# Optimization experiments

Measured on AMD Instinct MI355X. Metric: run time of the kernel, lower is better.

Reference implementation:

```python
import jax, jax.numpy as jnp
import numpy as np

N = 100000   # nodes
E = 1600000  # edges
D = 128      # input_dim
H = 128      # hidden_dim
G = 64       # graphs in batch
L = 3        # num GCN layers
BN_EPS = 1e-5


def setup_inputs() -> dict:
    key = jax.random.key(0)
    ks = jax.random.split(key, 16)
    s = 1.0 / np.sqrt(H)
    inp = {
        "x": jax.random.normal(ks[0], (N, D), jnp.float32),
        "edge_index": jax.random.randint(ks[1], (2, E), 0, N, dtype=jnp.int64),
        "batch": jnp.sort(jax.random.randint(ks[2], (N,), 0, G, dtype=jnp.int64)),
        # stacked GCNConv params (input_dim == hidden_dim so layer 0 stacks too)
        "conv_w": jax.random.normal(ks[3], (L, H, H), jnp.float32) * s,
        "conv_b": jax.random.normal(ks[4], (L, H), jnp.float32) * 0.01,
        # BatchNorm1d running stats + affine (eval mode)
        "bn_gamma": jnp.ones((L, H), jnp.float32),
        "bn_beta": jnp.zeros((L, H), jnp.float32),
        "bn_mean": jax.random.normal(ks[5], (L, H), jnp.float32) * 0.1,
        "bn_var": jax.random.uniform(ks[6], (L, H), jnp.float32, 0.5, 1.5),
        # node head MLP
        "node_w1": jax.random.normal(ks[7], (H // 2, H), jnp.float32) * s,
        "node_b1": jnp.zeros((H // 2,), jnp.float32),
        "node_w2": jax.random.normal(ks[8], (2, H // 2), jnp.float32) * (1.0 / np.sqrt(H // 2)),
        "node_b2": jnp.zeros((2,), jnp.float32),
        # graph head MLP
        "graph_w1": jax.random.normal(ks[9], (H // 2, H), jnp.float32) * s,
        "graph_b1": jnp.zeros((H // 2,), jnp.float32),
        "graph_w2": jax.random.normal(ks[10], (2, H // 2), jnp.float32) * (1.0 / np.sqrt(H // 2)),
        "graph_b2": jnp.zeros((2,), jnp.float32),
    }
    return inp


def _gcn_layer(h, src, dst, deg_inv_sqrt, w, b):
    # PyG GCNConv: h' = W h, then symmetric-normalized scatter-add over
    # edges (self-loops already appended to src/dst).
    h = h @ w.T                                   # [N, H]
    norm = deg_inv_sqrt[src] * deg_inv_sqrt[dst]  # [E+N]
    msg = h[src] * norm[:, None]                  # [E+N, H] gather
    out = jax.ops.segment_sum(msg, dst, num_segments=N)  # scatter-add
    return out + b


def _forward(x, edge_index, batch, conv_w, conv_b, bn_gamma, bn_beta,
             bn_mean, bn_var, node_w1, node_b1, node_w2, node_b2,
             graph_w1, graph_b1, graph_w2, graph_b2):
    loops = jnp.arange(N, dtype=edge_index.dtype)
    src = jnp.concatenate([edge_index[0], loops])
    dst = jnp.concatenate([edge_index[1], loops])
    deg = jax.ops.segment_sum(jnp.ones_like(src, dtype=x.dtype), dst,
                              num_segments=N)
    deg_inv_sqrt = jnp.where(deg > 0, jax.lax.rsqrt(deg), 0.0)

    h = x
    for i in range(L):  # conv -> BN(eval) -> ReLU (dropout inactive in eval)
        h = _gcn_layer(h, src, dst, deg_inv_sqrt, conv_w[i], conv_b[i])
        h = (h - bn_mean[i]) * jax.lax.rsqrt(bn_var[i] + BN_EPS) * bn_gamma[i] + bn_beta[i]
        h = jax.nn.relu(h)

    node_pred = jax.nn.relu(h @ node_w1.T + node_b1) @ node_w2.T + node_b2

    counts = jax.ops.segment_sum(jnp.ones((N,), h.dtype), batch,
                                 num_segments=G)
    graph_emb = jax.ops.segment_sum(h, batch, num_segments=G) / \
        jnp.maximum(counts, 1.0)[:, None]
    graph_pred = jax.nn.relu(graph_emb @ graph_w1.T + graph_b1) @ graph_w2.T + graph_b2
    return node_pred, graph_pred


def reference(x, edge_index, batch, conv_w, conv_b, bn_gamma, bn_beta,
              bn_mean, bn_var, node_w1, node_b1, node_w2, node_b2,
              graph_w1, graph_b1, graph_w2, graph_b2):
    return _forward(x, edge_index, batch, conv_w, conv_b, bn_gamma, bn_beta,
                    bn_mean, bn_var, node_w1, node_b1, node_w2, node_b2,
                    graph_w1, graph_b1, graph_w2, graph_b2)
```

## Files before the change

### kernel.cpp

```cpp
#include <hip/hip_runtime.h>
#include <hip/hip_bf16.h>

#define NN 100000
#define EE 1600000
#define HH 128
#define GG 64
#define LL 3
#define BN_EPS 1e-5f
#define NT 391
#define CHW 392
#define CAP 6144

typedef __hip_bfloat16 bf16;
typedef __attribute__((ext_vector_type(8))) short short8;
typedef __attribute__((ext_vector_type(4))) float floatx4;

__device__ __forceinline__ float lo16(unsigned v) { return __uint_as_float(v << 16); }
__device__ __forceinline__ float hi16(unsigned v) { return __uint_as_float(v & 0xffff0000u); }
__device__ __forceinline__ unsigned short f2b(float v) {
    bf16 h = __float2bfloat16(v);
    return *(unsigned short*)&h;
}
__device__ __forceinline__ unsigned pack2(float a, float b) {
    return (unsigned)f2b(a) | ((unsigned)f2b(b) << 16);
}
__device__ __forceinline__ int geti(const int* __restrict__ p, int i, int f) {
    return f ? p[2 * i] : p[i];
}

__global__ __launch_bounds__(1024) void k_part(const int* __restrict__ ei,
        unsigned* __restrict__ chunk, unsigned short* __restrict__ lbu,
        int* __restrict__ flag,
        const float* __restrict__ conv_w, const float* __restrict__ nw1,
        unsigned short* __restrict__ cwB, unsigned short* __restrict__ n1B,
        float* __restrict__ bnA, float* __restrict__ bnB,
        const float* __restrict__ conv_b, const float* __restrict__ g,
        const float* __restrict__ be, const float* __restrict__ mn,
        const float* __restrict__ vr, float* __restrict__ gsum,
        float* __restrict__ gcnt, unsigned* __restrict__ tbz) {
    __shared__ int lcnt[NT];
    __shared__ int wsum[8];
    __shared__ unsigned short lbs[CHW];
    __shared__ unsigned sorted[4096];
    int t = threadIdx.x;
    int e0 = blockIdx.x * 4096;
    int probe = ei[2 * (e0 + (t & 63)) + 1];
    int f = __any(probe != 0) ? 0 : 1;
    if (blockIdx.x == 0 && t == 0) *flag = f;
    int gi = blockIdx.x * 1024 + t;
    if (gi < LL * HH * HH) cwB[gi] = f2b(conv_w[gi]);
    if (gi < 64 * HH) n1B[gi] = f2b(nw1[gi]);
    if (gi < LL * HH) {
        float A = g[gi] * rsqrtf(vr[gi] + BN_EPS);
        bnA[gi] = A;
        bnB[gi] = (conv_b[gi] - mn[gi]) * A + be[gi];
    }
    if (gi < GG * HH) gsum[gi] = 0.f;
    if (gi < GG) gcnt[gi] = 0.f;
    if (gi < 64) tbz[(size_t)NN * 64 + gi] = 0u;
    int nume = EE - e0 < 4096 ? EE - e0 : 4096;
    for (int i = t; i < NT; i += 1024) lcnt[i] = 0;
    __syncthreads();
    unsigned pk[4]; int ml[4], mt[4];
#pragma unroll
    for (int i = 0; i < 4; i++) {
        int li = i * 1024 + t;
        if (li < nume) {
            int e = e0 + li;
            int src = geti(ei, e, f), dst = geti(ei, EE + e, f);
            mt[i] = dst >> 8;
            pk[i] = ((unsigned)src << 8) | (unsigned)(dst & 255);
            ml[i] = atomicAdd(&lcnt[mt[i]], 1);
        }
    }
    __syncthreads();
    int own = 0, x = 0;
    if (t < 512) { own = t < NT ? lcnt[t] : 0; x = own; }
#pragma unroll
    for (int off = 1; off < 64; off <<= 1) {
        int y = __shfl_up(x, off);
        if ((t & 63) >= off) x += y;
    }
    if (t < 512 && (t & 63) == 63) wsum[t >> 6] = x;
    __syncthreads();
    if (t < NT) {
        int pre = 0, w = t >> 6;
#pragma unroll
        for (int i = 0; i < 7; i++) if (i < w) pre += wsum[i];
        lbs[t] = (unsigned short)(pre + x - own);
    }
    if (t == 0) lbs[NT] = (unsigned short)nume;
    __syncthreads();
#pragma unroll
    for (int i = 0; i < 4; i++) {
        int li = i * 1024 + t;
        if (li < nume) sorted[(int)lbs[mt[i]] + ml[i]] = pk[i];
    }
    if (t < CHW) lbu[blockIdx.x * CHW + t] = lbs[t];
    __syncthreads();
    for (int idx = t; idx < nume; idx += 1024)
        chunk[e0 + idx] = sorted[idx];
}

__global__ __launch_bounds__(1024) void k_csr(const unsigned* __restrict__ chunk,
        const unsigned short* __restrict__ lbu, unsigned* __restrict__ csr,
        int* __restrict__ offs, int* __restrict__ cnt, float* __restrict__ dinv) {
    __shared__ unsigned stage[CAP];
    __shared__ unsigned outb[CAP];
    __shared__ int wsum[8];
    __shared__ int w2[4];
    __shared__ int segso[512];
    __shared__ int segst[512];
    __shared__ int hist[256], cur[256];
    __shared__ int s_nep;
    int T = blockIdx.x, t = threadIdx.x;
    int st = 0, rl = 0;
    if (t < NT) {
        int s0 = lbu[t * CHW + T];
        int s1 = lbu[t * CHW + T + 1];
        st = t * 4096 + s0;
        rl = s1 - s0;
    }
    int x = (t < 512) ? rl : 0;
#pragma unroll
    for (int off = 1; off < 64; off <<= 1) {
        int y = __shfl_up(x, off);
        if ((t & 63) >= off) x += y;
    }
    if (t < 512 && (t & 63) == 63) wsum[t >> 6] = x;
    if (t < 256) hist[t] = 0;
    __syncthreads();
    int tot = 0;
#pragma unroll
    for (int i = 0; i < 8; i++) tot += wsum[i];
    int ne = tot > CAP ? CAP : tot;
    if (t < 512) {
        int pre = 0, w = t >> 6;
#pragma unroll
        for (int i = 0; i < 7; i++) if (i < w) pre += wsum[i];
        segso[t] = pre + x - rl;
        segst[t] = st;
    }
    __syncthreads();
    for (int i = t; i < ne; i += 1024) {
        int lo = 0;
#pragma unroll
        for (int b = 256; b; b >>= 1) {
            int nlo = lo + b;
            if (nlo < 512 && segso[nlo] <= i) lo = nlo;
        }
        stage[i] = chunk[segst[lo] + (i - segso[lo])];
    }
    __syncthreads();
    for (int i = t; i < ne; i += 1024)
        atomicAdd(&hist[stage[i] & 255u], 1);
    __syncthreads();
    int c = 0, pc = 0, x2 = 0;
    if (t < 256) {
        c = hist[t];
        pc = (c + 7) & ~7;
        x2 = pc;
    }
#pragma unroll
    for (int off = 1; off < 64; off <<= 1) {
        int y = __shfl_up(x2, off);
        if ((t & 63) >= off) x2 += y;
    }
    if (t < 256 && (t & 63) == 63) w2[t >> 6] = x2;
    __syncthreads();
    if (t < 256) {
        int pre = 0, w = t >> 6;
#pragma unroll
        for (int i = 0; i < 3; i++) if (i < w) pre += w2[i];
        int stn = pre + x2 - pc;
        cur[t] = stn;
        int node = T * 256 + t;
        if (node < NN) {
            offs[node] = T * CAP + stn;
            cnt[node] = c;
            dinv[node] = rsqrtf(1.0f + (float)c);
        }
        for (int i = stn + c; i < stn + pc && i < CAP; i++)
            outb[i] = NN;
    }
    if (t == 0) {
        int tt = w2[0] + w2[1] + w2[2] + w2[3];
        s_nep = tt < CAP ? tt : CAP;
    }
    __syncthreads();
    for (int i = t; i < ne; i += 1024) {
        unsigned p = stage[i];
        int q = atomicAdd(&cur[p & 255u], 1);
        if (q < CAP) outb[q] = p >> 8;
    }
    __syncthreads();
    int nep = s_nep;
    for (int i = t; i < nep; i += 1024)
        csr[(size_t)T * CAP + i] = outb[i];
}

template<typename AT, int NC, bool FUSE>
__global__ __launch_bounds__(256) void k_gemm(const AT* __restrict__ in,
        const unsigned short* __restrict__ Wb, const float* __restrict__ bias,
        unsigned short* __restrict__ outh, int do_relu,
        const float* __restrict__ scale,
        const float* __restrict__ w2, const float* __restrict__ b2v,
        float* __restrict__ out2f) {
    __shared__ char sB[NC * 272];
    int wave = threadIdx.x >> 6, lane = threadIdx.x & 63;
    int ln = lane & 15, q = lane >> 4;
    {
        const short8* wsrc = (const short8*)Wb;
        for (int i = threadIdx.x; i < NC * 16; i += 256) {
            short8 v = wsrc[i];
            *(short8*)(sB + (i >> 4) * 272 + (i & 15) * 16) = v;
        }
    }
    int r0 = blockIdx.x * 64 + wave * 16;
    int row = r0 + ln;
    int rr = row < NN ? row : NN - 1;
    short8 a[4];
    if constexpr (sizeof(AT) == 2) {
        const short8* ap = (const short8*)(in + (size_t)rr * HH);
#pragma unroll
        for (int kt = 0; kt < 4; kt++) a[kt] = ap[kt * 4 + q];
    } else {
        const float4* ap = (const float4*)(in + (size_t)rr * HH);
#pragma unroll
        for (int kt = 0; kt < 4; kt++) {
            float4 f0 = ap[(kt * 4 + q) * 2];
            float4 f1 = ap[(kt * 4 + q) * 2 + 1];
            a[kt][0] = (short)f2b(f0.x); a[kt][1] = (short)f2b(f0.y);
            a[kt][2] = (short)f2b(f0.z); a[kt][3] = (short)f2b(f0.w);
            a[kt][4] = (short)f2b(f1.x); a[kt][5] = (short)f2b(f1.y);
            a[kt][6] = (short)f2b(f1.z); a[kt][7] = (short)f2b(f1.w);
        }
    }
    float scl[4];
    if constexpr (!FUSE) {
#pragma unroll
        for (int reg = 0; reg < 4; reg++) {
            int orow = r0 + q * 4 + reg;
            scl[reg] = scale ? scale[orow < NN ? orow : NN - 1] : 1.f;
        }
    }
    __syncthreads();
    float p0[4], p1[4];
    if constexpr (FUSE) {
#pragma unroll
        for (int r = 0; r < 4; r++) { p0[r] = 0.f; p1[r] = 0.f; }
    }
#pragma unroll
    for (int ct = 0; ct < NC / 16; ct++) {
        int c = ct * 16 + ln;
        floatx4 acc = {0.f, 0.f, 0.f, 0.f};
#pragma unroll
        for (int kt = 0; kt < 4; kt++) {
            short8 b = *(const short8*)(sB + (size_t)c * 272 + kt * 64 + q * 16);
            acc = __builtin_amdgcn_mfma_f32_16x16x32_bf16(a[kt], b, acc, 0, 0, 0);
        }
        float bv = bias ? bias[c] : 0.f;
        if constexpr (FUSE) {
            float wa = w2[c], wb = w2[64 + c];
#pragma unroll
            for (int reg = 0; reg < 4; reg++) {
                float v = fmaxf(acc[reg] + bv, 0.f);
                p0[reg] = fmaf(v, wa, p0[reg]);
                p1[reg] = fmaf(v, wb, p1[reg]);
            }
        } else {
#pragma unroll
            for (int reg = 0; reg < 4; reg++) {
                int orow = r0 + q * 4 + reg;
                if (orow < NN) {
                    float v = acc[reg] + bv;
                    if (do_relu) v = fmaxf(v, 0.f);
                    outh[(size_t)orow * NC + c] = f2b(v * scl[reg]);
                }
            }
        }
    }
    if constexpr (FUSE) {
#pragma unroll
        for (int off = 1; off < 16; off <<= 1) {
#pragma unroll
            for (int r = 0; r < 4; r++) {
                p0[r] += __shfl_xor(p0[r], off);
                p1[r] += __shfl_xor(p1[r], off);
            }
        }
        if (ln == 0) {
            float ba = b2v[0], bb = b2v[1];
#pragma unroll
            for (int reg = 0; reg < 4; reg++) {
                int orow = r0 + q * 4 + reg;
                if (orow < NN)
                    ((float2*)out2f)[orow] = make_float2(p0[reg] + ba, p1[reg] + bb);
            }
        }
    }
}

__global__ __launch_bounds__(256) void k_aggr(const unsigned* __restrict__ tbs,
        const unsigned* __restrict__ csr, const int* __restrict__ offs,
        const int* __restrict__ cnt, const float* __restrict__ dinv,
        const float* __restrict__ bnA, const float* __restrict__ bnB,
        unsigned* __restrict__ hout) {
    int wave = threadIdx.x >> 6, lane = threadIdx.x & 63;
    int n0 = blockIdx.x * 8 + wave * 2;
    int n1 = n0 + 1;
    int base0 = __builtin_amdgcn_readfirstlane(offs[n0]);
    int base1 = __builtin_amdgcn_readfirstlane(offs[n1]);
    int ne0   = __builtin_amdgcn_readfirstlane(cnt[n0]);
    int ne1   = __builtin_amdgcn_readfirstlane(cnt[n1]);
    float dd0 = __uint_as_float(__builtin_amdgcn_readfirstlane(
                    (int)__float_as_uint(dinv[n0])));
    float dd1 = __uint_as_float(__builtin_amdgcn_readfirstlane(
                    (int)__float_as_uint(dinv[n1])));
    unsigned sv0 = tbs[(size_t)n0 * 64 + lane];
    unsigned sv1 = tbs[(size_t)n1 * 64 + lane];
    float ax0 = lo16(sv0), ay0 = hi16(sv0);
    float ax1 = lo16(sv1), ay1 = hi16(sv1);
    const unsigned* __restrict__ e0 = csr + base0;
    const unsigned* __restrict__ e1 = csr + base1;
    int nr0 = (ne0 + 7) & ~7, nr1 = (ne1 + 7) & ~7;
    int nr = nr0 > nr1 ? nr0 : nr1;
    for (int k0 = 0; k0 < nr; k0 += 8) {
        unsigned vv0[8], vv1[8];
        bool a0 = k0 < nr0, a1 = k0 < nr1;
        if (a0) {
#pragma unroll
            for (int j = 0; j < 8; j++) {
                int s = (int)e0[k0 + j];
                vv0[j] = tbs[(size_t)s * 64 + lane];
            }
        }
        if (a1) {
#pragma unroll
            for (int j = 0; j < 8; j++) {
                int s = (int)e1[k0 + j];
                vv1[j] = tbs[(size_t)s * 64 + lane];
            }
        }
        if (a0) {
#pragma unroll
            for (int j = 0; j < 8; j++) {
                ax0 += lo16(vv0[j]);
                ay0 += hi16(vv0[j]);
            }
        }
        if (a1) {
#pragma unroll
            for (int j = 0; j < 8; j++) {
                ax1 += lo16(vv1[j]);
                ay1 += hi16(vv1[j]);
            }
        }
    }
    float2 A = ((const float2*)bnA)[lane];
    float2 B = ((const float2*)bnB)[lane];
    float r0 = fmaxf(fmaf(ax0 * dd0, A.x, B.x), 0.f);
    float r1 = fmaxf(fmaf(ay0 * dd0, A.y, B.y), 0.f);
    float r2 = fmaxf(fmaf(ax1 * dd1, A.x, B.x), 0.f);
    float r3 = fmaxf(fmaf(ay1 * dd1, A.y, B.y), 0.f);
    hout[(size_t)n0 * 64 + lane] = pack2(r0, r1);
    hout[(size_t)n1 * 64 + lane] = pack2(r2, r3);
}

#define PN 32
__global__ __launch_bounds__(64) void k_pool(const unsigned* __restrict__ hb,
        const int* __restrict__ batch, float* __restrict__ gsum,
        float* __restrict__ gcnt, const int* __restrict__ flag) {
    int lane = threadIdx.x;
    int f = *flag;
    int s0 = blockIdx.x * PN;
    int cur = geti(batch, s0, f);
    float a0 = 0.f, a1 = 0.f, cn = 0.f;
    auto step = [&](int g, unsigned v) {
        if (g != cur) {
            atomicAdd(&gsum[cur * HH + 2 * lane], a0);
            atomicAdd(&gsum[cur * HH + 2 * lane + 1], a1);
            if (lane == 0) atomicAdd(&gcnt[cur], cn);
            a0 = a1 = cn = 0.f; cur = g;
        }
        a0 += lo16(v); a1 += hi16(v); cn += 1.f;
    };
    for (int n = s0; n < s0 + PN; n += 8) {
        int gg[8]; unsigned vv[8];
#pragma unroll
        for (int j = 0; j < 8; j++) {
            gg[j] = geti(batch, n + j, f);
            vv[j] = hb[(size_t)(n + j) * 64 + lane];
        }
#pragma unroll
        for (int j = 0; j < 8; j++) step(gg[j], vv[j]);
    }
    atomicAdd(&gsum[cur * HH + 2 * lane], a0);
    atomicAdd(&gsum[cur * HH + 2 * lane + 1], a1);
    if (lane == 0) atomicAdd(&gcnt[cur], cn);
}

__global__ __launch_bounds__(64) void k_ghead(const float* __restrict__ gsum,
        const float* __restrict__ gcnt, const float* __restrict__ w1,
        const float* __restrict__ b1, const float* __restrict__ w2,
        const float* __restrict__ b2v, float* __restrict__ out) {
    __shared__ float emb[HH];
    __shared__ float w1s[64 * 129];
    int g = blockIdx.x, lane = threadIdx.x;
    for (int gi = lane; gi < 64 * HH; gi += 64)
        w1s[(gi >> 7) * 129 + (gi & 127)] = w1[gi];
    float cn = gcnt[g];
    cn = cn > 1.f ? cn : 1.f;
    float inv = 1.f / cn;
    emb[lane] = gsum[g * HH + lane] * inv;
    emb[lane + 64] = gsum[g * HH + 64 + lane] * inv;
    __syncthreads();
    float acc = b1[lane];
    for (int k = 0; k < HH; k++) acc = fmaf(emb[k], w1s[lane * 129 + k], acc);
    float y = fmaxf(acc, 0.f);
    float v0 = y * w2[lane];
    float v1 = y * w2[64 + lane];
#pragma unroll
    for (int off = 32; off; off >>= 1) {
        v0 += __shfl_xor(v0, off);
        v1 += __shfl_xor(v1, off);
    }
    if (lane == 0) {
        out[(size_t)NN * 2 + g * 2]     = v0 + b2v[0];
        out[(size_t)NN * 2 + g * 2 + 1] = v1 + b2v[1];
    }
}

extern "C" void kernel_launch(void* const* d_in, const int* in_sizes, int n_in,
                              void* d_out, int out_size, void* d_ws, size_t ws_size,
                              hipStream_t stream) {
    const float* x      = (const float*)d_in[0];
    const int*   ei     = (const int*)d_in[1];
    const int*   batch  = (const int*)d_in[2];
    const float* conv_w = (const float*)d_in[3];
    const float* conv_b = (const float*)d_in[4];
    const float* bn_g   = (const float*)d_in[5];
    const float* bn_b   = (const float*)d_in[6];
    const float* bn_m   = (const float*)d_in[7];
    const float* bn_v   = (const float*)d_in[8];
    const float* nw1    = (const float*)d_in[9];
    const float* nb1    = (const float*)d_in[10];
    const float* nw2    = (const float*)d_in[11];
    const float* nb2    = (const float*)d_in[12];
    const float* gw1    = (const float*)d_in[13];
    const float* gb1    = (const float*)d_in[14];
    const float* gw2    = (const float*)d_in[15];
    const float* gb2    = (const float*)d_in[16];
    float* out = (float*)d_out;

    char* ws = (char*)d_ws;
    size_t off = 0;
    auto alloc = [&](size_t bytes) -> void* {
        void* p = ws + off;
        off += (bytes + 255) & ~(size_t)255;
        return p;
    };
    unsigned short* hb   = (unsigned short*)alloc((size_t)NN * HH * 2);
    unsigned short* tb   = (unsigned short*)alloc((size_t)(NN + 1) * HH * 2);
    unsigned* chunk  = (unsigned*)alloc((size_t)EE * 4);
    unsigned* csr    = (unsigned*)alloc((size_t)NT * CAP * 4);
    unsigned short* lbu = (unsigned short*)alloc((size_t)NT * CHW * 2);
    int*      offs   = (int*)     alloc((size_t)NN * 4);
    int*      cnt    = (int*)     alloc((size_t)NN * 4);
    float*    dinv   = (float*)   alloc((size_t)NN * 4);
    float*    bnA    = (float*)   alloc((size_t)LL * HH * 4);
    float*    bnB    = (float*)   alloc((size_t)LL * HH * 4);
    float*    gsum   = (float*)   alloc((size_t)GG * HH * 4);
    float*    gcnt   = (float*)   alloc((size_t)GG * 4);
    unsigned short* cwB = (unsigned short*)alloc((size_t)LL * HH * HH * 2);
    unsigned short* n1B = (unsigned short*)alloc((size_t)64 * HH * 2);
    int*      flag   = (int*)     alloc(256);

    k_part<<<NT, 1024, 0, stream>>>(ei, chunk, lbu, flag, conv_w, nw1, cwB, n1B,
            bnA, bnB, conv_b, bn_g, bn_b, bn_m, bn_v, gsum, gcnt, (unsigned*)tb);
    k_csr<<<NT, 1024, 0, stream>>>(chunk, lbu, csr, offs, cnt, dinv);

    k_gemm<float, HH, false><<<(NN + 63) / 64, 256, 0, stream>>>(
        x, cwB, nullptr, tb, 0, dinv, nullptr, nullptr, nullptr);
    k_aggr<<<NN / 8, 256, 0, stream>>>((const unsigned*)tb, csr, offs, cnt,
                                       dinv, bnA, bnB, (unsigned*)hb);
    for (int l = 1; l < LL; l++) {
        k_gemm<unsigned short, HH, false><<<(NN + 63) / 64, 256, 0, stream>>>(
            hb, cwB + (size_t)l * HH * HH, nullptr, tb, 0, dinv,
            nullptr, nullptr, nullptr);
        k_aggr<<<NN / 8, 256, 0, stream>>>((const unsigned*)tb, csr, offs,
                                           cnt, dinv, bnA + l * HH,
                                           bnB + l * HH, (unsigned*)hb);
    }

    k_gemm<unsigned short, 64, true><<<(NN + 63) / 64, 256, 0, stream>>>(
        hb, n1B, nb1, nullptr, 1, nullptr, nw2, nb2, out);

    k_pool<<<(NN + PN - 1) / PN, 64, 0, stream>>>((const unsigned*)hb, batch,
                                                  gsum, gcnt, flag);
    k_ghead<<<GG, 64, 0, stream>>>(gsum, gcnt, gw1, gb1, gw2, gb2, out);
}
```

Measured before the change: 411.4 us.

## Fuse all pipeline stages into one cooperative persistent kernel with grid syncs

Replaces the sequence of separate launches (partition, CSR build, per-layer GEMM and aggregation, node head, pooling, graph head) with a single cooperative kernel. The phases are separated by grid-wide barriers and each phase grid-strides over its tiles. The aim is to remove per-launch overhead and the gaps between kernels. In exchange it adds grid-sync cost, moves GEMM tiles to 1024-thread blocks, and sets a launch bound of 8 blocks of 1024 threads per CU. That bound can force a very low register budget and cause spills, and the phases lose per-kernel tuning.

```diff
diff --git a/kernel.cpp b/kernel.cpp
--- a/kernel.cpp
+++ b/kernel.cpp
@@ -1,5 +1,8 @@
 #include <hip/hip_runtime.h>
 #include <hip/hip_bf16.h>
+#include <hip/hip_cooperative_groups.h>
+
+namespace cg = cooperative_groups;
 
 #define NN 100000
 #define EE 1600000
@@ -10,6 +13,9 @@
 #define NT 391
 #define CHW 392
 #define CAP 6144
+#define PN 32
+#define NTG 391
+#define SMEM_BYTES 55552
 
 typedef __hip_bfloat16 bf16;
 typedef __attribute__((ext_vector_type(8))) short short8;
@@ -28,430 +34,470 @@
     return f ? p[2 * i] : p[i];
 }
 
-__global__ __launch_bounds__(1024) void k_part(const int* __restrict__ ei,
-        unsigned* __restrict__ chunk, unsigned short* __restrict__ lbu,
-        int* __restrict__ flag,
-        const float* __restrict__ conv_w, const float* __restrict__ nw1,
-        unsigned short* __restrict__ cwB, unsigned short* __restrict__ n1B,
-        float* __restrict__ bnA, float* __restrict__ bnB,
-        const float* __restrict__ conv_b, const float* __restrict__ g,
-        const float* __restrict__ be, const float* __restrict__ mn,
-        const float* __restrict__ vr, float* __restrict__ gsum,
-        float* __restrict__ gcnt, unsigned* __restrict__ tbz) {
-    __shared__ int lcnt[NT];
-    __shared__ int wsum[8];
-    __shared__ unsigned short lbs[CHW];
-    __shared__ unsigned sorted[4096];
+struct MegaArgs {
+    const int* ei; const int* batch; const float* x;
+    const float* conv_w; const float* conv_b;
+    const float* bn_g; const float* bn_b; const float* bn_m; const float* bn_v;
+    const float* nw1; const float* nb1; const float* nw2; const float* nb2;
+    const float* gw1; const float* gb1; const float* gw2; const float* gb2;
+    float* out;
+    unsigned short* hb; unsigned short* tb;
+    unsigned* chunk; unsigned* csr; unsigned short* lbu;
+    int* offs; int* cnt; float* dinv;
+    float* bnA; float* bnB; float* gsum; float* gcnt;
+    unsigned short* cwB; unsigned short* n1B; int* flag;
+};
+
+__device__ void phase_part(char* smem, int NB, int f, const MegaArgs& A) {
+    int* lcnt = (int*)smem;
+    int* wsum = (int*)(smem + 1568);
+    unsigned short* lbs = (unsigned short*)(smem + 1600);
+    unsigned* sorted = (unsigned*)(smem + 2384);
     int t = threadIdx.x;
-    int e0 = blockIdx.x * 4096;
-    int probe = ei[2 * (e0 + (t & 63)) + 1];
-    int f = __any(probe != 0) ? 0 : 1;
-    if (blockIdx.x == 0 && t == 0) *flag = f;
     int gi = blockIdx.x * 1024 + t;
-    if (gi < LL * HH * HH) cwB[gi] = f2b(conv_w[gi]);
-    if (gi < 64 * HH) n1B[gi] = f2b(nw1[gi]);
+    if (gi < LL * HH * HH) A.cwB[gi] = f2b(A.conv_w[gi]);
+    if (gi < 64 * HH) A.n1B[gi] = f2b(A.nw1[gi]);
     if (gi < LL * HH) {
-        float A = g[gi] * rsqrtf(vr[gi] + BN_EPS);
-        bnA[gi] = A;
-        bnB[gi] = (conv_b[gi] - mn[gi]) * A + be[gi];
-    }
-    if (gi < GG * HH) gsum[gi] = 0.f;
-    if (gi < GG) gcnt[gi] = 0.f;
-    if (gi < 64) tbz[(size_t)NN * 64 + gi] = 0u;
-    int nume = EE - e0 < 4096 ? EE - e0 : 4096;
-    for (int i = t; i < NT; i += 1024) lcnt[i] = 0;
-    __syncthreads();
-    unsigned pk[4]; int ml[4], mt[4];
-#pragma unroll
-    for (int i = 0; i < 4; i++) {
-        int li = i * 1024 + t;
-        if (li < nume) {
-            int e = e0 + li;
-            int src = geti(ei, e, f), dst = geti(ei, EE + e, f);
-            mt[i] = dst >> 8;
-            pk[i] = ((unsigned)src << 8) | (unsigned)(dst & 255);
-            ml[i] = atomicAdd(&lcnt[mt[i]], 1);
-        }
-    }
-    __syncthreads();
-    int own = 0, x = 0;
-    if (t < 512) { own = t < NT ? lcnt[t] : 0; x = own; }
-#pragma unroll
-    for (int off = 1; off < 64; off <<= 1) {
-        int y = __shfl_up(x, off);
-        if ((t & 63) >= off) x += y;
-    }
-    if (t < 512 && (t & 63) == 63) wsum[t >> 6] = x;
-    __syncthreads();
-    if (t < NT) {
-        int pre = 0, w = t >> 6;
-#pragma unroll
-        for (int i = 0; i < 7; i++) if (i < w) pre += wsum[i];
-        lbs[t] = (unsigned short)(pre + x - own);
-    }
-    if (t == 0) lbs[NT] = (unsigned short)nume;
-    __syncthreads();
-#pragma unroll
-    for (int i = 0; i < 4; i++) {
-        int li = i * 1024 + t;
-        if (li < nume) sorted[(int)lbs[mt[i]] + ml[i]] = pk[i];
-    }
-    if (t < CHW) lbu[blockIdx.x * CHW + t] = lbs[t];
-    __syncthreads();
-    for (int idx = t; idx < nume; idx += 1024)
-        chunk[e0 + idx] = sorted[idx];
-}
-
-__global__ __launch_bounds__(1024) void k_csr(const unsigned* __restrict__ chunk,
-        const unsigned short* __restrict__ lbu, unsigned* __restrict__ csr,
-        int* __restrict__ offs, int* __restrict__ cnt, float* __restrict__ dinv) {
-    __shared__ unsigned stage[CAP];
-    __shared__ unsigned outb[CAP];
-    __shared__ int wsum[8];
-    __shared__ int w2[4];
-    __shared__ int segso[512];
-    __shared__ int segst[512];
-    __shared__ int hist[256], cur[256];
-    __shared__ int s_nep;
-    int T = blockIdx.x, t = threadIdx.x;
-    int st = 0, rl = 0;
-    if (t < NT) {
-        int s0 = lbu[t * CHW + T];
-        int s1 = lbu[t * CHW + T + 1];
-        st = t * 4096 + s0;
-        rl = s1 - s0;
-    }
-    int x = (t < 512) ? rl : 0;
-#pragma unroll
-    for (int off = 1; off < 64; off <<= 1) {
-        int y = __shfl_up(x, off);
-        if ((t & 63) >= off) x += y;
-    }
-    if (t < 512 && (t & 63) == 63) wsum[t >> 6] = x;
-    if (t < 256) hist[t] = 0;
-    __syncthreads();
-    int tot = 0;
-#pragma unroll
-    for (int i = 0; i < 8; i++) tot += wsum[i];
-    int ne = tot > CAP ? CAP : tot;
-    if (t < 512) {
-        int pre = 0, w = t >> 6;
-#pragma unroll
-        for (int i = 0; i < 7; i++) if (i < w) pre += wsum[i];
-        segso[t] = pre + x - rl;
-        segst[t] = st;
-    }
-    __syncthreads();
-    for (int i = t; i < ne; i += 1024) {
-        int lo = 0;
-#pragma unroll
-        for (int b = 256; b; b >>= 1) {
-            int nlo = lo + b;
-            if (nlo < 512 && segso[nlo] <= i) lo = nlo;
-        }
-        stage[i] = chunk[segst[lo] + (i - segso[lo])];
-    }
-    __syncthreads();
-    for (int i = t; i < ne; i += 1024)
-        atomicAdd(&hist[stage[i] & 255u], 1);
-    __syncthreads();
-    int c = 0, pc = 0, x2 = 0;
-    if (t < 256) {
-        c = hist[t];
-        pc = (c + 7) & ~7;
-        x2 = pc;
-    }
-#pragma unroll
-    for (int off = 1; off < 64; off <<= 1) {
-        int y = __shfl_up(x2, off);
-        if ((t & 63) >= off) x2 += y;
-    }
-    if (t < 256 && (t & 63) == 63) w2[t >> 6] = x2;
-    __syncthreads();
-    if (t < 256) {
-        int pre = 0, w = t >> 6;
-#pragma unroll
-        for (int i = 0; i < 3; i++) if (i < w) pre += w2[i];
-        int stn = pre + x2 - pc;
-        cur[t] = stn;
-        int node = T * 256 + t;
-        if (node < NN) {
-            offs[node] = T * CAP + stn;
-            cnt[node] = c;
-            dinv[node] = rsqrtf(1.0f + (float)c);
-        }
-        for (int i = stn + c; i < stn + pc && i < CAP; i++)
-            outb[i] = NN;
-    }
-    if (t == 0) {
-        int tt = w2[0] + w2[1] + w2[2] + w2[3];
-        s_nep = tt < CAP ? tt : CAP;
-    }
-    __syncthreads();
-    for (int i = t; i < ne; i += 1024) {
-        unsigned p = stage[i];
-        int q = atomicAdd(&cur[p & 255u], 1);
-        if (q < CAP) outb[q] = p >> 8;
-    }
-    __syncthreads();
-    int nep = s_nep;
-    for (int i = t; i < nep; i += 1024)
-        csr[(size_t)T * CAP + i] = outb[i];
+        float Av = A.bn_g[gi] * rsqrtf(A.bn_v[gi] + BN_EPS);
+        A.bnA[gi] = Av;
+        A.bnB[gi] = (A.conv_b[gi] - A.bn_m[gi]) * Av + A.bn_b[gi];
+    }
+    if (gi < GG * HH) A.gsum[gi] = 0.f;
+    if (gi < GG) A.gcnt[gi] = 0.f;
+    if (gi < 64) ((unsigned*)A.tb)[(size_t)NN * 64 + gi] = 0u;
+    if (blockIdx.x == 0 && t == 0) *A.flag = f;
+    for (int T = blockIdx.x; T < NT; T += NB) {
+        int e0 = T * 4096;
+        int nume = EE - e0 < 4096 ? EE - e0 : 4096;
+        for (int i = t; i < NT; i += 1024) lcnt[i] = 0;
+        __syncthreads();
+        unsigned pk[4]; int ml[4], mt[4];
+#pragma unroll
+        for (int i = 0; i < 4; i++) {
+            int li = i * 1024 + t;
+            if (li < nume) {
+                int e = e0 + li;
+                int src = geti(A.ei, e, f), dst = geti(A.ei, EE + e, f);
+                mt[i] = dst >> 8;
+                pk[i] = ((unsigned)src << 8) | (unsigned)(dst & 255);
+                ml[i] = atomicAdd(&lcnt[mt[i]], 1);
+            }
+        }
+        __syncthreads();
+        int own = 0, x = 0;
+        if (t < 512) { own = t < NT ? lcnt[t] : 0; x = own; }
+#pragma unroll
+        for (int off = 1; off < 64; off <<= 1) {
+            int y = __shfl_up(x, off);
+            if ((t & 63) >= off) x += y;
+        }
+        if (t < 512 && (t & 63) == 63) wsum[t >> 6] = x;
+        __syncthreads();
+        if (t < NT) {
+            int pre = 0, w = t >> 6;
+#pragma unroll
+            for (int i = 0; i < 7; i++) if (i < w) pre += wsum[i];
+            lbs[t] = (unsigned short)(pre + x - own);
+        }
+        if (t == 0) lbs[NT] = (unsigned short)nume;
+        __syncthreads();
+#pragma unroll
+        for (int i = 0; i < 4; i++) {
+            int li = i * 1024 + t;
+            if (li < nume) sorted[(int)lbs[mt[i]] + ml[i]] = pk[i];
+        }
+        if (t < CHW) A.lbu[T * CHW + t] = lbs[t];
+        __syncthreads();
+        for (int idx = t; idx < nume; idx += 1024)
+            A.chunk[e0 + idx] = sorted[idx];
+    }
+}
+
+__device__ void phase_csr(char* smem, int NB, const MegaArgs& A) {
+    unsigned* stage = (unsigned*)smem;
+    unsigned* outb  = (unsigned*)(smem + 24576);
+    int* segso = (int*)(smem + 49152);
+    int* segst = (int*)(smem + 51200);
+    int* hist  = (int*)(smem + 53248);
+    int* cur   = (int*)(smem + 54272);
+    int* wsum  = (int*)(smem + 55296);
+    int* w2x   = (int*)(smem + 55328);
+    int* s_nep = (int*)(smem + 55344);
+    int t = threadIdx.x;
+    for (int T = blockIdx.x; T < NT; T += NB) {
+        int st = 0, rl = 0;
+        if (t < NT) {
+            int s0 = A.lbu[t * CHW + T];
+            int s1 = A.lbu[t * CHW + T + 1];
+            st = t * 4096 + s0;
+            rl = s1 - s0;
+        }
+        int x = (t < 512) ? rl : 0;
+#pragma unroll
+        for (int off = 1; off < 64; off <<= 1) {
+            int y = __shfl_up(x, off);
+            if ((t & 63) >= off) x += y;
+        }
+        if (t < 512 && (t & 63) == 63) wsum[t >> 6] = x;
+        if (t < 256) hist[t] = 0;
+        __syncthreads();
+        int tot = 0;
+#pragma unroll
+        for (int i = 0; i < 8; i++) tot += wsum[i];
+        int ne = tot > CAP ? CAP : tot;
+        if (t < 512) {
+            int pre = 0, w = t >> 6;
+#pragma unroll
+            for (int i = 0; i < 7; i++) if (i < w) pre += wsum[i];
+            segso[t] = pre + x - rl;
+            segst[t] = st;
+        }
+        __syncthreads();
+        for (int i = t; i < ne; i += 1024) {
+            int lo = 0;
+#pragma unroll
+            for (int b = 256; b; b >>= 1) {
+                int nlo = lo + b;
+                if (nlo < 512 && segso[nlo] <= i) lo = nlo;
+            }
+            stage[i] = A.chunk[segst[lo] + (i - segso[lo])];
+        }
+        __syncthreads();
+        for (int i = t; i < ne; i += 1024)
+            atomicAdd(&hist[stage[i] & 255u], 1);
+        __syncthreads();
+        int c = 0, pc = 0, x2 = 0;
+        if (t < 256) {
+            c = hist[t];
+            pc = (c + 7) & ~7;
+            x2 = pc;
+        }
+#pragma unroll
+        for (int off = 1; off < 64; off <<= 1) {
+            int y = __shfl_up(x2, off);
+            if ((t & 63) >= off) x2 += y;
+        }
+        if (t < 256 && (t & 63) == 63) w2x[t >> 6] = x2;
+        __syncthreads();
+        if (t < 256) {
+            int pre = 0, w = t >> 6;
+#pragma unroll
+            for (int i = 0; i < 3; i++) if (i < w) pre += w2x[i];
+            int stn = pre + x2 - pc;
+            cur[t] = stn;
+            int node = T * 256 + t;
+            if (node < NN) {
+                A.offs[node] = T * CAP + stn;
+                A.cnt[node] = c;
+                A.dinv[node] = rsqrtf(1.0f + (float)c);
+            }
+            for (int i = stn + c; i < stn + pc && i < CAP; i++)
+                outb[i] = NN;
+        }
+        if (t == 0) {
+            int tt = w2x[0] + w2x[1] + w2x[2] + w2x[3];
+            *s_nep = tt < CAP ? tt : CAP;
+        }
+        __syncthreads();
+        for (int i = t; i < ne; i += 1024) {
+            unsigned p = stage[i];
+            int q = atomicAdd(&cur[p & 255u], 1);
+            if (q < CAP) outb[q] = p >> 8;
+        }
+        __syncthreads();
+        int nep = *s_nep;
+        for (int i = t; i < nep; i += 1024)
+            A.csr[(size_t)T * CAP + i] = outb[i];
+        __syncthreads();
+    }
 }
 
 template<typename AT, int NC, bool FUSE>
-__global__ __launch_bounds__(256) void k_gemm(const AT* __restrict__ in,
+__device__ void phase_gemm(char* smem, int NB, const AT* __restrict__ in,
         const unsigned short* __restrict__ Wb, const float* __restrict__ bias,
         unsigned short* __restrict__ outh, int do_relu,
-        const float* __restrict__ scale,
-        const float* __restrict__ w2, const float* __restrict__ b2v,
-        float* __restrict__ out2f) {
-    __shared__ char sB[NC * 272];
-    int wave = threadIdx.x >> 6, lane = threadIdx.x & 63;
-    int ln = lane & 15, q = lane >> 4;
-    {
-        const short8* wsrc = (const short8*)Wb;
-        for (int i = threadIdx.x; i < NC * 16; i += 256) {
-            short8 v = wsrc[i];
-            *(short8*)(sB + (i >> 4) * 272 + (i & 15) * 16) = v;
-        }
-    }
-    int r0 = blockIdx.x * 64 + wave * 16;
-    int row = r0 + ln;
-    int rr = row < NN ? row : NN - 1;
-    short8 a[4];
-    if constexpr (sizeof(AT) == 2) {
-        const short8* ap = (const short8*)(in + (size_t)rr * HH);
-#pragma unroll
-        for (int kt = 0; kt < 4; kt++) a[kt] = ap[kt * 4 + q];
-    } else {
-        const float4* ap = (const float4*)(in + (size_t)rr * HH);
-#pragma unroll
-        for (int kt = 0; kt < 4; kt++) {
-            float4 f0 = ap[(kt * 4 + q) * 2];
-            float4 f1 = ap[(kt * 4 + q) * 2 + 1];
-            a[kt][0] = (short)f2b(f0.x); a[kt][1] = (short)f2b(f0.y);
-            a[kt][2] = (short)f2b(f0.z); a[kt][3] = (short)f2b(f0.w);
-            a[kt][4] = (short)f2b(f1.x); a[kt][5] = (short)f2b(f1.y);
-            a[kt][6] = (short)f2b(f1.z); a[kt][7] = (short)f2b(f1.w);
-        }
-    }
-    float scl[4];
-    if constexpr (!FUSE) {
-#pragma unroll
-        for (int reg = 0; reg < 4; reg++) {
-            int orow = r0 + q * 4 + reg;
-            scl[reg] = scale ? scale[orow < NN ? orow : NN - 1] : 1.f;
-        }
-    }
+        const float* __restrict__ scale, const float* __restrict__ w2,
+        const float* __restrict__ b2v, float* __restrict__ out2f) {
+    char* sB = smem;
+    int t = threadIdx.x;
+    int wave = t >> 6, lane = t & 63, ln = lane & 15, q = lane >> 4;
+    const short8* wsrc = (const short8*)Wb;
+    for (int i = t; i < NC * 16; i += 1024)
+        *(short8*)(sB + (i >> 4) * 272 + (i & 15) * 16) = wsrc[i];
     __syncthreads();
-    float p0[4], p1[4];
-    if constexpr (FUSE) {
-#pragma unroll
-        for (int r = 0; r < 4; r++) { p0[r] = 0.f; p1[r] = 0.f; }
-    }
-#pragma unroll
-    for (int ct = 0; ct < NC / 16; ct++) {
-        int c = ct * 16 + ln;
-        floatx4 acc = {0.f, 0.f, 0.f, 0.f};
-#pragma unroll
-        for (int kt = 0; kt < 4; kt++) {
-            short8 b = *(const short8*)(sB + (size_t)c * 272 + kt * 64 + q * 16);
-            acc = __builtin_amdgcn_mfma_f32_16x16x32_bf16(a[kt], b, acc, 0, 0, 0);
-        }
-        float bv = bias ? bias[c] : 0.f;
-        if constexpr (FUSE) {
-            float wa = w2[c], wb = w2[64 + c];
-#pragma unroll
-            for (int reg = 0; reg < 4; reg++) {
-                float v = fmaxf(acc[reg] + bv, 0.f);
-                p0[reg] = fmaf(v, wa, p0[reg]);
-                p1[reg] = fmaf(v, wb, p1[reg]);
-            }
+    for (int T = blockIdx.x; T < NTG; T += NB) {
+        int r0 = T * 256 + wave * 16;
+        int row = r0 + ln;
+        int rr = row < NN ? row : NN - 1;
+        short8 a[4];
+        if constexpr (sizeof(AT) == 2) {
+            const short8* ap = (const short8*)(in + (size_t)rr * HH);
+#pragma unroll
+            for (int kt = 0; kt < 4; kt++) a[kt] = ap[kt * 4 + q];
         } else {
+            const float4* ap = (const float4*)(in + (size_t)rr * HH);
+#pragma unroll
+            for (int kt = 0; kt < 4; kt++) {
+                float4 f0 = ap[(kt * 4 + q) * 2];
+                float4 f1 = ap[(kt * 4 + q) * 2 + 1];
+                a[kt][0] = (short)f2b(f0.x); a[kt][1] = (short)f2b(f0.y);
+                a[kt][2] = (short)f2b(f0.z); a[kt][3] = (short)f2b(f0.w);
+                a[kt][4] = (short)f2b(f1.x); a[kt][5] = (short)f2b(f1.y);
+                a[kt][6] = (short)f2b(f1.z); a[kt][7] = (short)f2b(f1.w);
+            }
+        }
+        float scl[4];
+        if constexpr (!FUSE) {
 #pragma unroll
             for (int reg = 0; reg < 4; reg++) {
                 int orow = r0 + q * 4 + reg;
-                if (orow < NN) {
-                    float v = acc[reg] + bv;
-                    if (do_relu) v = fmaxf(v, 0.f);
-                    outh[(size_t)orow * NC + c] = f2b(v * scl[reg]);
-                }
-            }
-        }
-    }
-    if constexpr (FUSE) {
-#pragma unroll
-        for (int off = 1; off < 16; off <<= 1) {
-#pragma unroll
-            for (int r = 0; r < 4; r++) {
-                p0[r] += __shfl_xor(p0[r], off);
-                p1[r] += __shfl_xor(p1[r], off);
-            }
-        }
-        if (ln == 0) {
-            float ba = b2v[0], bb = b2v[1];
-#pragma unroll
-            for (int reg = 0; reg < 4; reg++) {
-                int orow = r0 + q * 4 + reg;
-                if (orow < NN)
-                    ((float2*)out2f)[orow] = make_float2(p0[reg] + ba, p1[reg] + bb);
-            }
-        }
-    }
-}
-
-__global__ __launch_bounds__(256) void k_aggr(const unsigned* __restrict__ tbs,
+                scl[reg] = scale ? scale[orow < NN ? orow : NN - 1] : 1.f;
+            }
+        }
+        float p0[4], p1[4];
+        if constexpr (FUSE) {
+#pragma unroll
+            for (int r = 0; r < 4; r++) { p0[r] = 0.f; p1[r] = 0.f; }
+        }
+#pragma unroll
+        for (int ct = 0; ct < NC / 16; ct++) {
+            int c = ct * 16 + ln;
+            floatx4 acc = {0.f, 0.f, 0.f, 0.f};
+#pragma unroll
+            for (int kt = 0; kt < 4; kt++) {
+                short8 b = *(const short8*)(sB + (size_t)c * 272 + kt * 64 + q * 16);
+                acc = __builtin_amdgcn_mfma_f32_16x16x32_bf16(a[kt], b, acc, 0, 0, 0);
+            }
+            float bv = bias ? bias[c] : 0.f;
+            if constexpr (FUSE) {
+                float wa = w2[c], wb = w2[64 + c];
+#pragma unroll
+                for (int reg = 0; reg < 4; reg++) {
+                    float v = fmaxf(acc[reg] + bv, 0.f);
+                    p0[reg] = fmaf(v, wa, p0[reg]);
+                    p1[reg] = fmaf(v, wb, p1[reg]);
+                }
+            } else {
+#pragma unroll
+                for (int reg = 0; reg < 4; reg++) {
+                    int orow = r0 + q * 4 + reg;
+                    if (orow < NN) {
+                        float v = acc[reg] + bv;
+                        if (do_relu) v = fmaxf(v, 0.f);
+                        outh[(size_t)orow * NC + c] = f2b(v * scl[reg]);
+                    }
+                }
+            }
+        }
+        if constexpr (FUSE) {
+#pragma unroll
+            for (int off = 1; off < 16; off <<= 1) {
+#pragma unroll
+                for (int r = 0; r < 4; r++) {
+                    p0[r] += __shfl_xor(p0[r], off);
+                    p1[r] += __shfl_xor(p1[r], off);
+                }
+            }
+            if (ln == 0) {
+                float ba = b2v[0], bb = b2v[1];
+#pragma unroll
+                for (int reg = 0; reg < 4; reg++) {
+                    int orow = r0 + q * 4 + reg;
+                    if (orow < NN)
+                        ((float2*)out2f)[orow] = make_float2(p0[reg] + ba, p1[reg] + bb);
+                }
+            }
+        }
+    }
+}
+
+__device__ void phase_aggr(int NB, const unsigned* __restrict__ tbs,
         const unsigned* __restrict__ csr, const int* __restrict__ offs,
         const int* __restrict__ cnt, const float* __restrict__ dinv,
         const float* __restrict__ bnA, const float* __restrict__ bnB,
         unsigned* __restrict__ hout) {
-    int wave = threadIdx.x >> 6, lane = threadIdx.x & 63;
-    int n0 = blockIdx.x * 8 + wave * 2;
-    int n1 = n0 + 1;
-    int base0 = __builtin_amdgcn_readfirstlane(offs[n0]);
-    int base1 = __builtin_amdgcn_readfirstlane(offs[n1]);
-    int ne0   = __builtin_amdgcn_readfirstlane(cnt[n0]);
-    int ne1   = __builtin_amdgcn_readfirstlane(cnt[n1]);
-    float dd0 = __uint_as_float(__builtin_amdgcn_readfirstlane(
-                    (int)__float_as_uint(dinv[n0])));
-    float dd1 = __uint_as_float(__builtin_amdgcn_readfirstlane(
-                    (int)__float_as_uint(dinv[n1])));
-    unsigned sv0 = tbs[(size_t)n0 * 64 + lane];
-    unsigned sv1 = tbs[(size_t)n1 * 64 + lane];
-    float ax0 = lo16(sv0), ay0 = hi16(sv0);
-    float ax1 = lo16(sv1), ay1 = hi16(sv1);
-    const unsigned* __restrict__ e0 = csr + base0;
-    const unsigned* __restrict__ e1 = csr + base1;
-    int nr0 = (ne0 + 7) & ~7, nr1 = (ne1 + 7) & ~7;
-    int nr = nr0 > nr1 ? nr0 : nr1;
-    for (int k0 = 0; k0 < nr; k0 += 8) {
-        unsigned vv0[8], vv1[8];
-        bool a0 = k0 < nr0, a1 = k0 < nr1;
-        if (a0) {
+    int t = threadIdx.x, wave = t >> 6, lane = t & 63;
+    for (int cid = blockIdx.x; cid < NN / 32; cid += NB) {
+        int n0 = cid * 32 + wave * 2;
+        int n1 = n0 + 1;
+        int base0 = __builtin_amdgcn_readfirstlane(offs[n0]);
+        int base1 = __builtin_amdgcn_readfirstlane(offs[n1]);
+        int ne0   = __builtin_amdgcn_readfirstlane(cnt[n0]);
+        int ne1   = __builtin_amdgcn_readfirstlane(cnt[n1]);
+        float dd0 = __uint_as_float(__builtin_amdgcn_readfirstlane(
+                        (int)__float_as_uint(dinv[n0])));
+        float dd1 = __uint_as_float(__builtin_amdgcn_readfirstlane(
+                        (int)__float_as_uint(dinv[n1])));
+        unsigned sv0 = tbs[(size_t)n0 * 64 + lane];
+        unsigned sv1 = tbs[(size_t)n1 * 64 + lane];
+        float ax0 = lo16(sv0), ay0 = hi16(sv0);
+        float ax1 = lo16(sv1), ay1 = hi16(sv1);
+        const unsigned* __restrict__ e0 = csr + base0;
+        const unsigned* __restrict__ e1 = csr + base1;
+        int nr0 = (ne0 + 7) & ~7, nr1 = (ne1 + 7) & ~7;
+        int nr = nr0 > nr1 ? nr0 : nr1;
+        for (int k0 = 0; k0 < nr; k0 += 8) {
+            unsigned vv0[8], vv1[8];
+            bool a0 = k0 < nr0, a1 = k0 < nr1;
+            if (a0) {
+#pragma unroll
+                for (int j = 0; j < 8; j++) {
+                    int s = (int)e0[k0 + j];
+                    vv0[j] = tbs[(size_t)s * 64 + lane];
+                }
+            }
+            if (a1) {
+#pragma unroll
+                for (int j = 0; j < 8; j++) {
+                    int s = (int)e1[k0 + j];
+                    vv1[j] = tbs[(size_t)s * 64 + lane];
+                }
+            }
+            if (a0) {
+#pragma unroll
+                for (int j = 0; j < 8; j++) {
+                    ax0 += lo16(vv0[j]);
+                    ay0 += hi16(vv0[j]);
+                }
+            }
+            if (a1) {
+#pragma unroll
+                for (int j = 0; j < 8; j++) {
+                    ax1 += lo16(vv1[j]);
+                    ay1 += hi16(vv1[j]);
+                }
+            }
+        }
+        float2 Av = ((const float2*)bnA)[lane];
+        float2 Bv = ((const float2*)bnB)[lane];
+        float r0 = fmaxf(fmaf(ax0 * dd0, Av.x, Bv.x), 0.f);
+        float r1 = fmaxf(fmaf(ay0 * dd0, Av.y, Bv.y), 0.f);
+        float r2 = fmaxf(fmaf(ax1 * dd1, Av.x, Bv.x), 0.f);
+        float r3 = fmaxf(fmaf(ay1 * dd1, Av.y, Bv.y), 0.f);
+        hout[(size_t)n0 * 64 + lane] = pack2(r0, r1);
+        hout[(size_t)n1 * 64 + lane] = pack2(r2, r3);
+    }
+}
+
+__device__ void phase_pool(int NB, int f, const unsigned* __restrict__ hb,
+        const int* __restrict__ batch, float* __restrict__ gsum,
+        float* __restrict__ gcnt) {
+    int t = threadIdx.x, wave = t >> 6, lane = t & 63;
+    for (int cid = blockIdx.x * 16 + wave; cid < NN / PN; cid += NB * 16) {
+        int s0 = cid * PN;
+        int cur = geti(batch, s0, f);
+        float a0 = 0.f, a1 = 0.f, cn = 0.f;
+        auto step = [&](int g, unsigned v) {
+            if (g != cur) {
+                atomicAdd(&gsum[cur * HH + 2 * lane], a0);
+                atomicAdd(&gsum[cur * HH + 2 * lane + 1], a1);
+                if (lane == 0) atomicAdd(&gcnt[cur], cn);
+                a0 = a1 = cn = 0.f; cur = g;
+            }
+            a0 += lo16(v); a1 += hi16(v); cn += 1.f;
+        };
+        for (int n = s0; n < s0 + PN; n += 8) {
+            int gg[8]; unsigned vv[8];
 #pragma unroll
             for (int j = 0; j < 8; j++) {
-                int s = (int)e0[k0 + j];
-                vv0[j] = tbs[(size_t)s * 64 + lane];
-            }
-        }
-        if (a1) {
-#pragma unroll
-            for (int j = 0; j < 8; j++) {
-                int s = (int)e1[k0 + j];
-                vv1[j] = tbs[(size_t)s * 64 + lane];
-            }
-        }
-        if (a0) {
-#pragma unroll
-            for (int j = 0; j < 8; j++) {
-                ax0 += lo16(vv0[j]);
-                ay0 += hi16(vv0[j]);
-            }
-        }
-        if (a1) {
-#pragma unroll
-            for (int j = 0; j < 8; j++) {
-                ax1 += lo16(vv1[j]);
-                ay1 += hi16(vv1[j]);
-            }
-        }
-    }
-    float2 A = ((const float2*)bnA)[lane];
-    float2 B = ((const float2*)bnB)[lane];
-    float r0 = fmaxf(fmaf(ax0 * dd0, A.x, B.x), 0.f);
-    float r1 = fmaxf(fmaf(ay0 * dd0, A.y, B.y), 0.f);
-    float r2 = fmaxf(fmaf(ax1 * dd1, A.x, B.x), 0.f);
-    float r3 = fmaxf(fmaf(ay1 * dd1, A.y, B.y), 0.f);
-    hout[(size_t)n0 * 64 + lane] = pack2(r0, r1);
-    hout[(size_t)n1 * 64 + lane] = pack2(r2, r3);
-}
-
-#define PN 32
-__global__ __launch_bounds__(64) void k_pool(const unsigned* __restrict__ hb,
-        const int* __restrict__ batch, float* __restrict__ gsum,
-        float* __restrict__ gcnt, const int* __restrict__ flag) {
-    int lane = threadIdx.x;
-    int f = *flag;
-    int s0 = blockIdx.x * PN;
-    int cur = geti(batch, s0, f);
-    float a0 = 0.f, a1 = 0.f, cn = 0.f;
-    auto step = [&](int g, unsigned v) {
-        if (g != cur) {
-            atomicAdd(&gsum[cur * HH + 2 * lane], a0);
-            atomicAdd(&gsum[cur * HH + 2 * lane + 1], a1);
-            if (lane == 0) atomicAdd(&gcnt[cur], cn);
-            a0 = a1 = cn = 0.f; cur = g;
-        }
-        a0 += lo16(v); a1 += hi16(v); cn += 1.f;
-    };
-    for (int n = s0; n < s0 + PN; n += 8) {
-        int gg[8]; unsigned vv[8];
-#pragma unroll
-        for (int j = 0; j < 8; j++) {
-            gg[j] = geti(batch, n + j, f);
-            vv[j] = hb[(size_t)(n + j) * 64 + lane];
-        }
-#pragma unroll
-        for (int j = 0; j < 8; j++) step(gg[j], vv[j]);
-    }
-    atomicAdd(&gsum[cur * HH + 2 * lane], a0);
-    atomicAdd(&gsum[cur * HH + 2 * lane + 1], a1);
-    if (lane == 0) atomicAdd(&gcnt[cur], cn);
-}
-
-__global__ __launch_bounds__(64) void k_ghead(const float* __restrict__ gsum,
-        const float* __restrict__ gcnt, const float* __restrict__ w1,
-        const float* __restrict__ b1, const float* __restrict__ w2,
-        const float* __restrict__ b2v, float* __restrict__ out) {
-    __shared__ float emb[HH];
-    __shared__ float w1s[64 * 129];
-    int g = blockIdx.x, lane = threadIdx.x;
-    for (int gi = lane; gi < 64 * HH; gi += 64)
-        w1s[(gi >> 7) * 129 + (gi & 127)] = w1[gi];
-    float cn = gcnt[g];
-    cn = cn > 1.f ? cn : 1.f;
-    float inv = 1.f / cn;
-    emb[lane] = gsum[g * HH + lane] * inv;
-    emb[lane + 64] = gsum[g * HH + 64 + lane] * inv;
+                gg[j] = geti(batch, n + j, f);
+                vv[j] = hb[(size_t)(n + j) * 64 + lane];
+            }
+#pragma unroll
+            for (int j = 0; j < 8; j++) step(gg[j], vv[j]);
+        }
+        atomicAdd(&gsum[cur * HH + 2 * lane], a0);
+        atomicAdd(&gsum[cur * HH + 2 * lane + 1], a1);
+        if (lane == 0) atomicAdd(&gcnt[cur], cn);
+    }
+}
+
+__device__ void phase_ghead(char* smem, const MegaArgs& A) {
+    if (blockIdx.x >= GG) return;
+    float* w1s = (float*)smem;
+    float* emb = (float*)(smem + 33024);
+    int g = blockIdx.x, t = threadIdx.x;
+    for (int gi = t; gi < 64 * HH; gi += 1024)
+        w1s[(gi >> 7) * 129 + (gi & 127)] = A.gw1[gi];
+    if (t < HH) {
+        float cn = A.gcnt[g];
+        cn = cn > 1.f ? cn : 1.f;
+        emb[t] = A.gsum[g * HH + t] * (1.f / cn);
+    }
     __syncthreads();
-    float acc = b1[lane];
-    for (int k = 0; k < HH; k++) acc = fmaf(emb[k], w1s[lane * 129 + k], acc);
-    float y = fmaxf(acc, 0.f);
-    float v0 = y * w2[lane];
-    float v1 = y * w2[64 + lane];
-#pragma unroll
-    for (int off = 32; off; off >>= 1) {
-        v0 += __shfl_xor(v0, off);
-        v1 += __shfl_xor(v1, off);
-    }
-    if (lane == 0) {
-        out[(size_t)NN * 2 + g * 2]     = v0 + b2v[0];
-        out[(size_t)NN * 2 + g * 2 + 1] = v1 + b2v[1];
-    }
+    if (t < 64) {
+        float acc = A.gb1[t];
+        for (int k = 0; k < HH; k++) acc = fmaf(emb[k], w1s[t * 129 + k], acc);
+        float y = fmaxf(acc, 0.f);
+        float v0 = y * A.gw2[t];
+        float v1 = y * A.gw2[64 + t];
+#pragma unroll
+        for (int off = 32; off; off >>= 1) {
+            v0 += __shfl_xor(v0, off);
+            v1 += __shfl_xor(v1, off);
+        }
+        if (t == 0) {
+            A.out[(size_t)NN * 2 + g * 2]     = v0 + A.gb2[0];
+            A.out[(size_t)NN * 2 + g * 2 + 1] = v1 + A.gb2[1];
+        }
+    }
+}
+
+__global__ __launch_bounds__(1024, 8) void k_mega(MegaArgs A) {
+    __shared__ __align__(16) char smem[SMEM_BYTES];
+    cg::grid_group grid = cg::this_grid();
+    int NB = (int)gridDim.x;
+    int t = threadIdx.x;
+    int probe = A.ei[2 * (t & 63) + 1];
+    int f = __any(probe != 0) ? 0 : 1;
+    phase_part(smem, NB, f, A);
+    grid.sync();
+    phase_csr(smem, NB, A);
+    grid.sync();
+    phase_gemm<float, HH, false>(smem, NB, A.x, A.cwB, nullptr, A.tb, 0,
+                                 A.dinv, nullptr, nullptr, nullptr);
+    grid.sync();
+    phase_aggr(NB, (const unsigned*)A.tb, A.csr, A.offs, A.cnt, A.dinv,
+               A.bnA, A.bnB, (unsigned*)A.hb);
+    grid.sync();
+    for (int l = 1; l < LL; l++) {
+        phase_gemm<unsigned short, HH, false>(smem, NB, A.hb,
+            A.cwB + (size_t)l * HH * HH, nullptr, A.tb, 0, A.dinv,
+            nullptr, nullptr, nullptr);
+        grid.sync();
+        phase_aggr(NB, (const unsigned*)A.tb, A.csr, A.offs, A.cnt, A.dinv,
+                   A.bnA + l * HH, A.bnB + l * HH, (unsigned*)A.hb);
+        grid.sync();
+    }
+    phase_gemm<unsigned short, 64, true>(smem, NB, A.hb, A.n1B, A.nb1,
+        nullptr, 1, nullptr, A.nw2, A.nb2, A.out);
+    phase_pool(NB, f, (const unsigned*)A.hb, A.batch, A.gsum, A.gcnt);
+    grid.sync();
+    phase_ghead(smem, A);
 }
 
 extern "C" void kernel_launch(void* const* d_in, const int* in_sizes, int n_in,
                               void* d_out, int out_size, void* d_ws, size_t ws_size,
                               hipStream_t stream) {
-    const float* x      = (const float*)d_in[0];
-    const int*   ei     = (const int*)d_in[1];
-    const int*   batch  = (const int*)d_in[2];
-    const float* conv_w = (const float*)d_in[3];
-    const float* conv_b = (const float*)d_in[4];
-    const float* bn_g   = (const float*)d_in[5];
-    const float* bn_b   = (const float*)d_in[6];
-    const float* bn_m   = (const float*)d_in[7];
-    const float* bn_v   = (const float*)d_in[8];
-    const float* nw1    = (const float*)d_in[9];
-    const float* nb1    = (const float*)d_in[10];
-    const float* nw2    = (const float*)d_in[11];
-    const float* nb2    = (const float*)d_in[12];
-    const float* gw1    = (const float*)d_in[13];
-    const float* gb1    = (const float*)d_in[14];
-    const float* gw2    = (const float*)d_in[15];
-    const float* gb2    = (const float*)d_in[16];
-    float* out = (float*)d_out;
+    MegaArgs ma;
+    ma.ei     = (const int*)d_in[1];
+    ma.batch  = (const int*)d_in[2];
+    ma.x      = (const float*)d_in[0];
+    ma.conv_w = (const float*)d_in[3];
+    ma.conv_b = (const float*)d_in[4];
+    ma.bn_g   = (const float*)d_in[5];
+    ma.bn_b   = (const float*)d_in[6];
+    ma.bn_m   = (const float*)d_in[7];
+    ma.bn_v   = (const float*)d_in[8];
+    ma.nw1    = (const float*)d_in[9];
+    ma.nb1    = (const float*)d_in[10];
+    ma.nw2    = (const float*)d_in[11];
+    ma.nb2    = (const float*)d_in[12];
+    ma.gw1    = (const float*)d_in[13];
+    ma.gb1    = (const float*)d_in[14];
+    ma.gw2    = (const float*)d_in[15];
+    ma.gb2    = (const float*)d_in[16];
+    ma.out    = (float*)d_out;
 
     char* ws = (char*)d_ws;
     size_t off = 0;
@@ -460,43 +506,28 @@
         off += (bytes + 255) & ~(size_t)255;
         return p;
     };
-    unsigned short* hb   = (unsigned short*)alloc((size_t)NN * HH * 2);
-    unsigned short* tb   = (unsigned short*)alloc((size_t)(NN + 1) * HH * 2);
-    unsigned* chunk  = (unsigned*)alloc((size_t)EE * 4);
-    unsigned* csr    = (unsigned*)alloc((size_t)NT * CAP * 4);
-    unsigned short* lbu = (unsigned short*)alloc((size_t)NT * CHW * 2);
-    int*      offs   = (int*)     alloc((size_t)NN * 4);
-    int*      cnt    = (int*)     alloc((size_t)NN * 4);
-    float*    dinv   = (float*)   alloc((size_t)NN * 4);
-    float*    bnA    = (float*)   alloc((size_t)LL * HH * 4);
-    float*    bnB    = (float*)   alloc((size_t)LL * HH * 4);
-    float*    gsum   = (float*)   alloc((size_t)GG * HH * 4);
-    float*    gcnt   = (float*)   alloc((size_t)GG * 4);
-    unsigned short* cwB = (unsigned short*)alloc((size_t)LL * HH * HH * 2);
-    unsigned short* n1B = (unsigned short*)alloc((size_t)64 * HH * 2);
-    int*      flag   = (int*)     alloc(256);
-
-    k_part<<<NT, 1024, 0, stream>>>(ei, chunk, lbu, flag, conv_w, nw1, cwB, n1B,
-            bnA, bnB, conv_b, bn_g, bn_b, bn_m, bn_v, gsum, gcnt, (unsigned*)tb);
-    k_csr<<<NT, 1024, 0, stream>>>(chunk, lbu, csr, offs, cnt, dinv);
-
-    k_gemm<float, HH, false><<<(NN + 63) / 64, 256, 0, stream>>>(
-        x, cwB, nullptr, tb, 0, dinv, nullptr, nullptr, nullptr);
-    k_aggr<<<NN / 8, 256, 0, stream>>>((const unsigned*)tb, csr, offs, cnt,
-                                       dinv, bnA, bnB, (unsigned*)hb);
-    for (int l = 1; l < LL; l++) {
-        k_gemm<unsigned short, HH, false><<<(NN + 63) / 64, 256, 0, stream>>>(
-            hb, cwB + (size_t)l * HH * HH, nullptr, tb, 0, dinv,
-            nullptr, nullptr, nullptr);
-        k_aggr<<<NN / 8, 256, 0, stream>>>((const unsigned*)tb, csr, offs,
-                                           cnt, dinv, bnA + l * HH,
-                                           bnB + l * HH, (unsigned*)hb);
-    }
-
-    k_gemm<unsigned short, 64, true><<<(NN + 63) / 64, 256, 0, stream>>>(
-        hb, n1B, nb1, nullptr, 1, nullptr, nw2, nb2, out);
-
-    k_pool<<<(NN + PN - 1) / PN, 64, 0, stream>>>((const unsigned*)hb, batch,
-                                                  gsum, gcnt, flag);
-    k_ghead<<<GG, 64, 0, stream>>>(gsum, gcnt, gw1, gb1, gw2, gb2, out);
-}
+    ma.hb    = (unsigned short*)alloc((size_t)NN * HH * 2);
+    ma.tb    = (unsigned short*)alloc((size_t)(NN + 1) * HH * 2);
+    ma.chunk = (unsigned*)alloc((size_t)EE * 4);
+    ma.csr   = (unsigned*)alloc((size_t)NT * CAP * 4);
+    ma.lbu   = (unsigned short*)alloc((size_t)NT * CHW * 2);
+    ma.offs  = (int*)alloc((size_t)NN * 4);
+    ma.cnt   = (int*)alloc((size_t)NN * 4);
+    ma.dinv  = (float*)alloc((size_t)NN * 4);
+    ma.bnA   = (float*)alloc((size_t)LL * HH * 4);
+    ma.bnB   = (float*)alloc((size_t)LL * HH * 4);
+    ma.gsum  = (float*)alloc((size_t)GG * HH * 4);
+    ma.gcnt  = (float*)alloc((size_t)GG * 4);
+    ma.cwB   = (unsigned short*)alloc((size_t)LL * HH * HH * 2);
+    ma.n1B   = (unsigned short*)alloc((size_t)64 * HH * 2);
+    ma.flag  = (int*)alloc(256);
+
+    int occ = 0;
+    hipOccupancyMaxActiveBlocksPerMultiprocessor(&occ, k_mega, 1024, 0);
+    if (occ < 1) occ = 1;
+    if (occ > 2) occ = 2;
+    int nb = occ * 256;
+    void* kargs[] = { (void*)&ma };
+    hipLaunchCooperativeKernel((void*)k_mega, dim3(nb), dim3(1024), kargs,
+                               0, stream);
+}
```

Result: slower. 890.4 us (+116.4%).
